# Kernel tuning notes

Measured on AMD Instinct MI355X. Metric: run time of the kernel, lower is better.

The kernel has to match this reference:

```python
import jax, jax.numpy as jnp
import numpy as np

EPS = 1e-5
NUM_GROUPS = 32


def setup_inputs() -> dict:
    key = jax.random.key(0)
    B, C, H, W = 16, 512, 32, 32
    ks = jax.random.split(key, 5)
    s = 1.0 / np.sqrt(C)  # keep attention logits well-scaled
    return {
        "x": jax.random.normal(ks[0], (B, C, H, W), jnp.float32),
        "gamma": jnp.ones((C,), jnp.float32),
        "beta": jnp.zeros((C,), jnp.float32),
        "wq": jax.random.normal(ks[1], (C, C), jnp.float32) * s,
        "bq": jnp.zeros((C,), jnp.float32),
        "wk": jax.random.normal(ks[2], (C, C), jnp.float32) * s,
        "bk": jnp.zeros((C,), jnp.float32),
        "wv": jax.random.normal(ks[3], (C, C), jnp.float32) * s,
        "bv": jnp.zeros((C,), jnp.float32),
        "wp": jax.random.normal(ks[4], (C, C), jnp.float32) * s,
        "bp": jnp.zeros((C,), jnp.float32),
    }


def _group_norm(x, gamma, beta):
    B, C, H, W = x.shape
    g = NUM_GROUPS
    xg = x.reshape(B, g, C // g, H * W)
    mu = jnp.mean(xg, axis=(2, 3), keepdims=True)
    var = jnp.mean(jnp.square(xg - mu), axis=(2, 3), keepdims=True)
    h = (xg - mu) * jax.lax.rsqrt(var + EPS)
    h = h.reshape(B, C, H, W)
    return h * gamma[None, :, None, None] + beta[None, :, None, None]


def reference(x, gamma, beta, wq, bq, wk, bk, wv, bv, wp, bp):
    B, C, H, W = x.shape
    N = H * W
    h = _group_norm(x, gamma, beta).reshape(B, C, N)  # [B,C,N]
    # 1x1 convs == per-pixel matmuls over channels
    q = jnp.einsum('oc,bcn->bon', wq, h) + bq[None, :, None]
    k = jnp.einsum('oc,bcn->bon', wk, h) + bk[None, :, None]
    v = jnp.einsum('oc,bcn->bon', wv, h) + bv[None, :, None]
    scale = int(C) ** (-0.5)
    logits = jnp.einsum('bcn,bcm->bnm', q, k) * scale  # [B,N,N]
    attn = jax.nn.softmax(logits, axis=-1)
    o = jnp.einsum('bnm,bcm->bcn', attn, v)  # [B,C,N]
    out = jnp.einsum('oc,bcn->bon', wp, o) + bp[None, :, None]
    return x + out.reshape(B, C, H, W)
```

## Files before the change

### kernel.cpp

```cpp
#include <hip/hip_runtime.h>
#include <hip/hip_bf16.h>

typedef __attribute__((ext_vector_type(8))) short bf16x8;
typedef __attribute__((ext_vector_type(4))) float f32x4;
typedef __attribute__((ext_vector_type(8))) unsigned short u16x8;
typedef __attribute__((ext_vector_type(4))) unsigned short u16x4;

static __device__ __forceinline__ unsigned short f2bf(float f) {
  __hip_bfloat16 h = __float2bfloat16(f);
  union { __hip_bfloat16 h; unsigned short u; } cv; cv.h = h; return cv.u;
}
static __device__ __forceinline__ float bf2f(unsigned short u) {
  union { unsigned int u; float f; } cv; cv.u = ((unsigned int)u) << 16; return cv.f;
}

static __device__ __forceinline__ void gload16(const unsigned short* g, unsigned short* l) {
  __builtin_amdgcn_global_load_lds((const __attribute__((address_space(1))) void*)g,
                                   (__attribute__((address_space(3))) void*)l, 16, 0, 0);
}

#define BK 32

__global__ __launch_bounds__(256, 4) void gemm_bt(
    const unsigned short* __restrict__ A, const unsigned short* __restrict__ Bm,
    long sA, long sB, int lda, int ldb, int K,
    const float* __restrict__ bias, int bias_mode, float post_scale,
    unsigned short* __restrict__ D, long sD, int ldd)
{
  __shared__ unsigned short lA[2][128 * BK];
  __shared__ unsigned short lB[2][128 * BK];
  const int gx = gridDim.x, gy = gridDim.y;
  const int nwg = gx * gy * gridDim.z;
  int orig = blockIdx.x + gx * (blockIdx.y + gy * blockIdx.z);
  int id = (orig & 7) * (nwg >> 3) + (orig >> 3);
  const int bxi = id % gx;
  int rem = id / gx;
  const int byi = rem % gy;
  const int bz = rem / gy;

  const int tid = threadIdx.x, lane = tid & 63, wid = tid >> 6;
  const int l15 = lane & 15, lhi = lane >> 4;
  const int wr = wid >> 1, wc = wid & 1;
  const long bm = (long)byi * 128, bn = (long)bxi * 128;
  const unsigned short* Ab = A + (size_t)bz * sA + (size_t)bm * lda;
  const unsigned short* Bb = Bm + (size_t)bz * sB + (size_t)bn * ldb;
  const int NT = K >> 5;

  f32x4 acc[4][4];
  #pragma unroll
  for (int i = 0; i < 4; ++i)
    #pragma unroll
    for (int j = 0; j < 4; ++j) acc[i][j] = (f32x4){0.f, 0.f, 0.f, 0.f};

  auto stage = [&](int buf, int k0) {
    #pragma unroll
    for (int j = 0; j < 2; ++j) {
      int bi = j * 256 + tid;
      int row = bi >> 2, sl = bi & 3;
      int kb = sl ^ ((row >> 1) & 3);
      gload16(Ab + (size_t)row * lda + k0 + kb * 8, &lA[buf][(j * 256 + wid * 64) * 8]);
    }
    #pragma unroll
    for (int j = 0; j < 2; ++j) {
      int bi = j * 256 + tid;
      int row = bi >> 2, sl = bi & 3;
      int kb = sl ^ ((row >> 1) & 3);
      gload16(Bb + (size_t)row * ldb + k0 + kb * 8, &lB[buf][(j * 256 + wid * 64) * 8]);
    }
  };

  stage(0, 0);
  __syncthreads();
  int buf = 0;
  for (int t = 0; t < NT; ++t) {
    if (t + 1 < NT) stage(buf ^ 1, (t + 1) * BK);
    bf16x8 af[4], bfr[4];
    #pragma unroll
    for (int mi = 0; mi < 4; ++mi) {
      int row = wr * 64 + mi * 16 + l15;
      int sl = lhi ^ ((row >> 1) & 3);
      af[mi] = *(const bf16x8*)&lA[buf][row * BK + sl * 8];
    }
    #pragma unroll
    for (int ni = 0; ni < 4; ++ni) {
      int row = wc * 64 + ni * 16 + l15;
      int sl = lhi ^ ((row >> 1) & 3);
      bfr[ni] = *(const bf16x8*)&lB[buf][row * BK + sl * 8];
    }
    #pragma unroll
    for (int mi = 0; mi < 4; ++mi)
      #pragma unroll
      for (int ni = 0; ni < 4; ++ni)
        acc[mi][ni] = __builtin_amdgcn_mfma_f32_16x16x32_bf16(af[mi], bfr[ni], acc[mi][ni], 0, 0, 0);
    __syncthreads();
    buf ^= 1;
  }

  #pragma unroll
  for (int mi = 0; mi < 4; ++mi) {
    #pragma unroll
    for (int ni = 0; ni < 4; ++ni) {
      #pragma unroll
      for (int r = 0; r < 4; ++r) {
        long row = bm + wr * 64 + mi * 16 + lhi * 4 + r;
        long col = bn + wc * 64 + ni * 16 + l15;
        float v = acc[mi][ni][r];
        if (bias_mode == 1) v += bias[row];
        else if (bias_mode == 2) v += bias[col];
        v *= post_scale;
        D[(size_t)bz * sD + (size_t)row * ldd + col] = f2bf(v);
      }
    }
  }
}

__global__ __launch_bounds__(256) void groupnorm_to_ht(
    const float* __restrict__ x, const float* __restrict__ gamma,
    const float* __restrict__ beta, unsigned short* __restrict__ ht)
{
  const int b = blockIdx.x >> 5;
  const int g = blockIdx.x & 31;
  const int tid = threadIdx.x, lane = tid & 63, wid = tid >> 6;
  const float4* xg4 = (const float4*)(x + ((size_t)b * 512 + g * 16) * 1024);
  float4 v[16];
  float s = 0.f, ss = 0.f;
  #pragma unroll
  for (int j = 0; j < 16; ++j) {
    v[j] = xg4[j * 256 + tid];
    s += v[j].x + v[j].y + v[j].z + v[j].w;
    ss += v[j].x * v[j].x + v[j].y * v[j].y + v[j].z * v[j].z + v[j].w * v[j].w;
  }
  #pragma unroll
  for (int o = 32; o; o >>= 1) { s += __shfl_xor(s, o); ss += __shfl_xor(ss, o); }
  __shared__ float red[8];
  if (lane == 0) { red[wid] = s; red[4 + wid] = ss; }
  __syncthreads();
  s = red[0] + red[1] + red[2] + red[3];
  ss = red[4] + red[5] + red[6] + red[7];
  const float mu = s * (1.f / 16384.f);
  const float var = ss * (1.f / 16384.f) - mu * mu;
  const float rsig = rsqrtf(var + 1e-5f);
  __shared__ unsigned short tile[16][1024];
  #pragma unroll
  for (int j = 0; j < 16; ++j) {
    int e = (j * 256 + tid) * 4;
    int ci = e >> 10, n = e & 1023;
    float ga = gamma[g * 16 + ci] * rsig, be = beta[g * 16 + ci];
    u16x4 o = { f2bf((v[j].x - mu) * ga + be), f2bf((v[j].y - mu) * ga + be),
                f2bf((v[j].z - mu) * ga + be), f2bf((v[j].w - mu) * ga + be) };
    *(u16x4*)&tile[ci][n] = o;
  }
  __syncthreads();
  unsigned short* hb = ht + (size_t)b * 1024 * 512 + g * 16;
  for (int rep = 0; rep < 4; ++rep) {
    int n = rep * 256 + tid;
    u16x8 lo, hi;
    #pragma unroll
    for (int ci = 0; ci < 8; ++ci) lo[ci] = tile[ci][n];
    #pragma unroll
    for (int ci = 0; ci < 8; ++ci) hi[ci] = tile[8 + ci][n];
    *(u16x8*)&hb[(size_t)n * 512] = lo;
    *(u16x8*)&hb[(size_t)n * 512 + 8] = hi;
  }
}

__global__ __launch_bounds__(256) void softmax_rows(unsigned short* __restrict__ attn)
{
  int row = blockIdx.x * 4 + (threadIdx.x >> 6);
  int lane = threadIdx.x & 63;
  unsigned short* p = attn + (size_t)row * 1024;
  u16x8 c0 = *(const u16x8*)&p[lane * 8];
  u16x8 c1 = *(const u16x8*)&p[512 + lane * 8];
  float f[16];
  #pragma unroll
  for (int j = 0; j < 8; ++j) { f[j] = bf2f(c0[j]); f[8 + j] = bf2f(c1[j]); }
  float m = f[0];
  #pragma unroll
  for (int j = 1; j < 16; ++j) m = fmaxf(m, f[j]);
  #pragma unroll
  for (int o = 32; o; o >>= 1) m = fmaxf(m, __shfl_xor(m, o));
  float sum = 0.f;
  #pragma unroll
  for (int j = 0; j < 16; ++j) { f[j] = __expf(f[j] - m); sum += f[j]; }
  #pragma unroll
  for (int o = 32; o; o >>= 1) sum += __shfl_xor(sum, o);
  float inv = 1.0f / sum;
  #pragma unroll
  for (int j = 0; j < 8; ++j) { c0[j] = f2bf(f[j] * inv); c1[j] = f2bf(f[8 + j] * inv); }
  *(u16x8*)&p[lane * 8] = c0;
  *(u16x8*)&p[512 + lane * 8] = c1;
}

__global__ __launch_bounds__(256) void residual_add(
    const float* __restrict__ x, const unsigned short* __restrict__ po,
    float* __restrict__ out)
{
  int t = blockIdx.x * 256 + threadIdx.x;
  int idx = t * 8;
  int b = idx >> 19, c = (idx >> 10) & 511, n = idx & 1023;
  u16x8 g = *(const u16x8*)&po[(size_t)c * 16384 + b * 1024 + n];
  float4 x0 = *(const float4*)&x[idx];
  float4 x1 = *(const float4*)&x[idx + 4];
  float4 o0 = { x0.x + bf2f(g[0]), x0.y + bf2f(g[1]), x0.z + bf2f(g[2]), x0.w + bf2f(g[3]) };
  float4 o1 = { x1.x + bf2f(g[4]), x1.y + bf2f(g[5]), x1.z + bf2f(g[6]), x1.w + bf2f(g[7]) };
  *(float4*)&out[idx] = o0;
  *(float4*)&out[idx + 4] = o1;
}

__global__ __launch_bounds__(256) void convert_weights(
    const float* __restrict__ wq, const float* __restrict__ wk,
    const float* __restrict__ wv, const float* __restrict__ wp,
    const float* __restrict__ bq, const float* __restrict__ bk,
    unsigned short* __restrict__ out, float* __restrict__ bqk)
{
  if (blockIdx.x == 1024) {
    int i = threadIdx.x * 4;
    if (i < 512) *(float4*)&bqk[i] = *(const float4*)&bq[i];
    else         *(float4*)&bqk[i] = *(const float4*)&bk[i - 512];
    return;
  }
  int t = blockIdx.x * 256 + threadIdx.x;
  int m = t >> 16;
  int off = (t & 65535) * 4;
  const float* src = m == 0 ? wq : m == 1 ? wk : m == 2 ? wv : wp;
  float4 v = *(const float4*)&src[off];
  u16x4 o = { f2bf(v.x), f2bf(v.y), f2bf(v.z), f2bf(v.w) };
  *(u16x4*)&out[(size_t)m * 262144 + off] = o;
}

extern "C" void kernel_launch(void* const* d_in, const int* in_sizes, int n_in,
                              void* d_out, int out_size, void* d_ws, size_t ws_size,
                              hipStream_t stream)
{
  const float* x     = (const float*)d_in[0];
  const float* gamma = (const float*)d_in[1];
  const float* beta  = (const float*)d_in[2];
  const float* wq    = (const float*)d_in[3];
  const float* bq    = (const float*)d_in[4];
  const float* wk    = (const float*)d_in[5];
  const float* bk    = (const float*)d_in[6];
  const float* wv    = (const float*)d_in[7];
  const float* bv    = (const float*)d_in[8];
  const float* wp    = (const float*)d_in[9];
  const float* bp    = (const float*)d_in[10];

  unsigned short* ws   = (unsigned short*)d_ws;
  unsigned short* w_bf = ws;
  unsigned short* ht   = w_bf + 1048576;
  unsigned short* qk   = ht + 8388608;
  unsigned short* vv2  = qk + 16777216;
  unsigned short* attn = vv2 + 8388608;
  unsigned short* ot   = attn + 16777216;
  float*          bqk  = (float*)(ot + 8388608);
  unsigned short* po   = attn;

  const float scale = 0.044194173824159216f;

  convert_weights<<<dim3(1025), dim3(256), 0, stream>>>(wq, wk, wv, wp, bq, bk, w_bf, bqk);
  groupnorm_to_ht<<<dim3(512), dim3(256), 0, stream>>>(x, gamma, beta, ht);

  gemm_bt<<<dim3(8, 128, 1), dim3(256), 0, stream>>>(
      ht, w_bf, 0L, 0L, 512, 512, 512,
      bqk, 2, 1.0f, qk, 0L, 1024);
  gemm_bt<<<dim3(128, 4, 1), dim3(256), 0, stream>>>(
      w_bf + 2 * 262144, ht, 0L, 0L, 512, 512, 512,
      bv, 1, 1.0f, vv2, 0L, 16384);
  gemm_bt<<<dim3(8, 8, 16), dim3(256), 0, stream>>>(
      qk, qk + 512, 1048576L, 1048576L, 1024, 1024, 512,
      (const float*)nullptr, 0, scale, attn, 1048576L, 1024);
  softmax_rows<<<dim3(4096), dim3(256), 0, stream>>>(attn);
  gemm_bt<<<dim3(4, 8, 16), dim3(256), 0, stream>>>(
      attn, vv2, 1048576L, 1024L, 1024, 16384, 1024,
      (const float*)nullptr, 0, 1.0f, ot, 524288L, 512);
  gemm_bt<<<dim3(128, 4, 1), dim3(256), 0, stream>>>(
      w_bf + 3 * 262144, ot, 0L, 0L, 512, 512, 512,
      bp, 1, 1.0f, po, 0L, 16384);
  residual_add<<<dim3(4096), dim3(256), 0, stream>>>(x, po, (float*)d_out);
}
```

Baseline: 185.7 us.

## Deepen GEMM pipeline to 4 stages, stage epilogue via LDS, fuse residual

The GEMM moves from a double-buffered LDS pipeline to a 4-slot ring in dynamic shared memory (64 KB), keeping three tiles in flight. It uses explicit vmcnt waits with a single barrier per iteration, aiming to hide global-load latency. Outputs are first staged through LDS so global stores are coalesced 16-byte writes. The final projection GEMM writes fp32 output with the residual added directly, which removes the separate residual_add kernel and the bf16 round-trip of the projection output. The larger LDS footprint lowers occupancy (launch bounds drop to 2 blocks per CU), and the hand-counted vmcnt values are fragile.

```diff
diff --git a/kernel.cpp b/kernel.cpp
--- a/kernel.cpp
+++ b/kernel.cpp
@@ -20,15 +20,16 @@
 }
 
 #define BK 32
-
-__global__ __launch_bounds__(256, 4) void gemm_bt(
+#define EPW 134
+
+__global__ __launch_bounds__(256, 2) void gemm_bt(
     const unsigned short* __restrict__ A, const unsigned short* __restrict__ Bm,
     long sA, long sB, int lda, int ldb, int K,
     const float* __restrict__ bias, int bias_mode, float post_scale,
-    unsigned short* __restrict__ D, long sD, int ldd)
-{
-  __shared__ unsigned short lA[2][128 * BK];
-  __shared__ unsigned short lB[2][128 * BK];
+    int out_mode, void* __restrict__ D, long sD, int ldd,
+    const float* __restrict__ resid)
+{
+  extern __shared__ unsigned short smem[];
   const int gx = gridDim.x, gy = gridDim.y;
   const int nwg = gx * gy * gridDim.z;
   int orig = blockIdx.x + gx * (blockIdx.y + gy * blockIdx.z);
@@ -52,64 +53,117 @@
     #pragma unroll
     for (int j = 0; j < 4; ++j) acc[i][j] = (f32x4){0.f, 0.f, 0.f, 0.f};
 
-  auto stage = [&](int buf, int k0) {
+  auto stage = [&](int t) {
+    const int slot = t & 3;
+    const int k0 = t * BK;
     #pragma unroll
     for (int j = 0; j < 2; ++j) {
       int bi = j * 256 + tid;
       int row = bi >> 2, sl = bi & 3;
       int kb = sl ^ ((row >> 1) & 3);
-      gload16(Ab + (size_t)row * lda + k0 + kb * 8, &lA[buf][(j * 256 + wid * 64) * 8]);
+      gload16(Ab + (size_t)row * lda + k0 + kb * 8,
+              &smem[slot * 8192 + (j * 256 + wid * 64) * 8]);
     }
     #pragma unroll
     for (int j = 0; j < 2; ++j) {
       int bi = j * 256 + tid;
       int row = bi >> 2, sl = bi & 3;
       int kb = sl ^ ((row >> 1) & 3);
-      gload16(Bb + (size_t)row * ldb + k0 + kb * 8, &lB[buf][(j * 256 + wid * 64) * 8]);
+      gload16(Bb + (size_t)row * ldb + k0 + kb * 8,
+              &smem[slot * 8192 + 4096 + (j * 256 + wid * 64) * 8]);
     }
   };
 
-  stage(0, 0);
-  __syncthreads();
-  int buf = 0;
+  stage(0); stage(1); stage(2);
+
   for (int t = 0; t < NT; ++t) {
-    if (t + 1 < NT) stage(buf ^ 1, (t + 1) * BK);
+    const int ahead = NT - 1 - t;
+    if (ahead >= 2)      asm volatile("s_waitcnt vmcnt(8)" ::: "memory");
+    else if (ahead == 1) asm volatile("s_waitcnt vmcnt(4)" ::: "memory");
+    else                 asm volatile("s_waitcnt vmcnt(0)" ::: "memory");
+    asm volatile("s_waitcnt lgkmcnt(0)" ::: "memory");
+    __builtin_amdgcn_s_barrier();
+    asm volatile("" ::: "memory");
+
+    const int slot = t & 3;
     bf16x8 af[4], bfr[4];
     #pragma unroll
     for (int mi = 0; mi < 4; ++mi) {
       int row = wr * 64 + mi * 16 + l15;
       int sl = lhi ^ ((row >> 1) & 3);
-      af[mi] = *(const bf16x8*)&lA[buf][row * BK + sl * 8];
+      af[mi] = *(const bf16x8*)&smem[slot * 8192 + row * BK + sl * 8];
     }
     #pragma unroll
     for (int ni = 0; ni < 4; ++ni) {
       int row = wc * 64 + ni * 16 + l15;
       int sl = lhi ^ ((row >> 1) & 3);
-      bfr[ni] = *(const bf16x8*)&lB[buf][row * BK + sl * 8];
-    }
+      bfr[ni] = *(const bf16x8*)&smem[slot * 8192 + 4096 + row * BK + sl * 8];
+    }
+    if (t + 3 < NT) stage(t + 3);
     #pragma unroll
     for (int mi = 0; mi < 4; ++mi)
       #pragma unroll
       for (int ni = 0; ni < 4; ++ni)
         acc[mi][ni] = __builtin_amdgcn_mfma_f32_16x16x32_bf16(af[mi], bfr[ni], acc[mi][ni], 0, 0, 0);
+  }
+  __syncthreads();
+
+  if (out_mode == 0) {
+    #pragma unroll
+    for (int mi = 0; mi < 4; ++mi) {
+      #pragma unroll
+      for (int ni = 0; ni < 4; ++ni) {
+        #pragma unroll
+        for (int r = 0; r < 4; ++r) {
+          int rl = wr * 64 + mi * 16 + lhi * 4 + r;
+          int cl = wc * 64 + ni * 16 + l15;
+          float v = acc[mi][ni][r];
+          if (bias_mode == 1) v += bias[bm + rl];
+          else if (bias_mode == 2) v += bias[bn + cl];
+          v *= post_scale;
+          smem[rl * EPW + cl] = f2bf(v);
+        }
+      }
+    }
     __syncthreads();
-    buf ^= 1;
-  }
-
-  #pragma unroll
-  for (int mi = 0; mi < 4; ++mi) {
-    #pragma unroll
-    for (int ni = 0; ni < 4; ++ni) {
+    const int row = tid >> 1, hf = tid & 1;
+    unsigned short* dst = (unsigned short*)D + (size_t)bz * sD + (size_t)(bm + row) * ldd + bn + hf * 64;
+    const unsigned short* src = &smem[row * EPW + hf * 64];
+    #pragma unroll
+    for (int j = 0; j < 8; ++j) *(u16x8*)&dst[j * 8] = *(const u16x8*)&src[j * 8];
+  } else {
+    float* smf = (float*)smem;
+    float* outF = (float*)D;
+    #pragma unroll
+    for (int h = 0; h < 2; ++h) {
+      if (wr == h) {
+        #pragma unroll
+        for (int mi = 0; mi < 4; ++mi)
+          #pragma unroll
+          for (int ni = 0; ni < 4; ++ni)
+            #pragma unroll
+            for (int r = 0; r < 4; ++r) {
+              int rl = mi * 16 + lhi * 4 + r;
+              int cl = wc * 64 + ni * 16 + l15;
+              float v = acc[mi][ni][r];
+              if (bias_mode == 1) v += bias[bm + h * 64 + rl];
+              smf[rl * EPW + cl] = v * post_scale;
+            }
+      }
+      __syncthreads();
+      const int rl = tid >> 2, q = tid & 3;
+      const long rowg = bm + h * 64 + rl;
       #pragma unroll
-      for (int r = 0; r < 4; ++r) {
-        long row = bm + wr * 64 + mi * 16 + lhi * 4 + r;
-        long col = bn + wc * 64 + ni * 16 + l15;
-        float v = acc[mi][ni][r];
-        if (bias_mode == 1) v += bias[row];
-        else if (bias_mode == 2) v += bias[col];
-        v *= post_scale;
-        D[(size_t)bz * sD + (size_t)row * ldd + col] = f2bf(v);
+      for (int j = 0; j < 8; ++j) {
+        long col = bn + q * 32 + j * 4;
+        long b = col >> 10, n = col & 1023;
+        size_t oi = (size_t)b * 524288 + (size_t)rowg * 1024 + n;
+        float4 v = *(const float4*)&smf[rl * EPW + q * 32 + j * 4];
+        float4 xr = *(const float4*)&resid[oi];
+        float4 o = { v.x + xr.x, v.y + xr.y, v.z + xr.z, v.w + xr.w };
+        *(float4*)&outF[oi] = o;
       }
+      __syncthreads();
     }
   }
 }
@@ -189,22 +243,6 @@
   for (int j = 0; j < 8; ++j) { c0[j] = f2bf(f[j] * inv); c1[j] = f2bf(f[8 + j] * inv); }
   *(u16x8*)&p[lane * 8] = c0;
   *(u16x8*)&p[512 + lane * 8] = c1;
-}
-
-__global__ __launch_bounds__(256) void residual_add(
-    const float* __restrict__ x, const unsigned short* __restrict__ po,
-    float* __restrict__ out)
-{
-  int t = blockIdx.x * 256 + threadIdx.x;
-  int idx = t * 8;
-  int b = idx >> 19, c = (idx >> 10) & 511, n = idx & 1023;
-  u16x8 g = *(const u16x8*)&po[(size_t)c * 16384 + b * 1024 + n];
-  float4 x0 = *(const float4*)&x[idx];
-  float4 x1 = *(const float4*)&x[idx + 4];
-  float4 o0 = { x0.x + bf2f(g[0]), x0.y + bf2f(g[1]), x0.z + bf2f(g[2]), x0.w + bf2f(g[3]) };
-  float4 o1 = { x1.x + bf2f(g[4]), x1.y + bf2f(g[5]), x1.z + bf2f(g[6]), x1.w + bf2f(g[7]) };
-  *(float4*)&out[idx] = o0;
-  *(float4*)&out[idx + 4] = o1;
 }
 
 __global__ __launch_bounds__(256) void convert_weights(
@@ -252,28 +290,29 @@
   unsigned short* attn = vv2 + 8388608;
   unsigned short* ot   = attn + 16777216;
   float*          bqk  = (float*)(ot + 8388608);
-  unsigned short* po   = attn;
 
   const float scale = 0.044194173824159216f;
+  const int SMEM = 65536;
+  hipFuncSetAttribute(reinterpret_cast<const void*>(&gemm_bt),
+                      hipFuncAttributeMaxDynamicSharedMemorySize, SMEM);
 
   convert_weights<<<dim3(1025), dim3(256), 0, stream>>>(wq, wk, wv, wp, bq, bk, w_bf, bqk);
   groupnorm_to_ht<<<dim3(512), dim3(256), 0, stream>>>(x, gamma, beta, ht);
 
-  gemm_bt<<<dim3(8, 128, 1), dim3(256), 0, stream>>>(
+  gemm_bt<<<dim3(8, 128, 1), dim3(256), SMEM, stream>>>(
       ht, w_bf, 0L, 0L, 512, 512, 512,
-      bqk, 2, 1.0f, qk, 0L, 1024);
-  gemm_bt<<<dim3(128, 4, 1), dim3(256), 0, stream>>>(
+      bqk, 2, 1.0f, 0, (void*)qk, 0L, 1024, (const float*)nullptr);
+  gemm_bt<<<dim3(128, 4, 1), dim3(256), SMEM, stream>>>(
       w_bf + 2 * 262144, ht, 0L, 0L, 512, 512, 512,
-      bv, 1, 1.0f, vv2, 0L, 16384);
-  gemm_bt<<<dim3(8, 8, 16), dim3(256), 0, stream>>>(
+      bv, 1, 1.0f, 0, (void*)vv2, 0L, 16384, (const float*)nullptr);
+  gemm_bt<<<dim3(8, 8, 16), dim3(256), SMEM, stream>>>(
       qk, qk + 512, 1048576L, 1048576L, 1024, 1024, 512,
-      (const float*)nullptr, 0, scale, attn, 1048576L, 1024);
+      (const float*)nullptr, 0, scale, 0, (void*)attn, 1048576L, 1024, (const float*)nullptr);
   softmax_rows<<<dim3(4096), dim3(256), 0, stream>>>(attn);
-  gemm_bt<<<dim3(4, 8, 16), dim3(256), 0, stream>>>(
+  gemm_bt<<<dim3(4, 8, 16), dim3(256), SMEM, stream>>>(
       attn, vv2, 1048576L, 1024L, 1024, 16384, 1024,
-      (const float*)nullptr, 0, 1.0f, ot, 524288L, 512);
-  gemm_bt<<<dim3(128, 4, 1), dim3(256), 0, stream>>>(
+      (const float*)nullptr, 0, 1.0f, 0, (void*)ot, 524288L, 512, (const float*)nullptr);
+  gemm_bt<<<dim3(128, 4, 1), dim3(256), SMEM, stream>>>(
       w_bf + 3 * 262144, ot, 0L, 0L, 512, 512, 512,
-      bp, 1, 1.0f, po, 0L, 16384);
-  residual_add<<<dim3(4096), dim3(256), 0, stream>>>(x, po, (float*)d_out);
-}
+      bp, 1, 1.0f, 1, d_out, 0L, 16384, x);
+}
```

After: 206.1 us. 11.0% more time.

## Load GEMM MFMA fragments directly from global memory, bypassing LDS staging

Applied to the files above, without the earlier changes.

The GEMM kernel drops its double-buffered LDS staging and __syncthreads barriers. Each wave now loads its A/B bf16 fragments straight from global memory into registers, using a two-deep register ping-pong to overlap loads with MFMA. This removes LDS traffic and block-wide synchronization. The cost is that wave pairs sharing rows load the same data twice from global/L2, plus higher register pressure (occupancy hint lowered from 4 to 3). The loop also assumes an even K/32 tile count.

```diff
diff --git a/kernel.cpp b/kernel.cpp
--- a/kernel.cpp
+++ b/kernel.cpp
@@ -14,21 +14,12 @@
   union { unsigned int u; float f; } cv; cv.u = ((unsigned int)u) << 16; return cv.f;
 }
 
-static __device__ __forceinline__ void gload16(const unsigned short* g, unsigned short* l) {
-  __builtin_amdgcn_global_load_lds((const __attribute__((address_space(1))) void*)g,
-                                   (__attribute__((address_space(3))) void*)l, 16, 0, 0);
-}
-
-#define BK 32
-
-__global__ __launch_bounds__(256, 4) void gemm_bt(
+__global__ __launch_bounds__(256, 3) void gemm_bt(
     const unsigned short* __restrict__ A, const unsigned short* __restrict__ Bm,
     long sA, long sB, int lda, int ldb, int K,
     const float* __restrict__ bias, int bias_mode, float post_scale,
     unsigned short* __restrict__ D, long sD, int ldd)
 {
-  __shared__ unsigned short lA[2][128 * BK];
-  __shared__ unsigned short lB[2][128 * BK];
   const int gx = gridDim.x, gy = gridDim.y;
   const int nwg = gx * gy * gridDim.z;
   int orig = blockIdx.x + gx * (blockIdx.y + gy * blockIdx.z);
@@ -42,9 +33,12 @@
   const int l15 = lane & 15, lhi = lane >> 4;
   const int wr = wid >> 1, wc = wid & 1;
   const long bm = (long)byi * 128, bn = (long)bxi * 128;
-  const unsigned short* Ab = A + (size_t)bz * sA + (size_t)bm * lda;
-  const unsigned short* Bb = Bm + (size_t)bz * sB + (size_t)bn * ldb;
-  const int NT = K >> 5;
+
+  const unsigned short* Abase = A + (size_t)bz * sA
+      + (size_t)(bm + wr * 64 + l15) * lda + lhi * 8;
+  const unsigned short* Bbase = Bm + (size_t)bz * sB
+      + (size_t)(bn + wc * 64 + l15) * ldb + lhi * 8;
+  const long lda16 = 16L * lda, ldb16 = 16L * ldb;
 
   f32x4 acc[4][4];
   #pragma unroll
@@ -52,48 +46,31 @@
     #pragma unroll
     for (int j = 0; j < 4; ++j) acc[i][j] = (f32x4){0.f, 0.f, 0.f, 0.f};
 
-  auto stage = [&](int buf, int k0) {
-    #pragma unroll
-    for (int j = 0; j < 2; ++j) {
-      int bi = j * 256 + tid;
-      int row = bi >> 2, sl = bi & 3;
-      int kb = sl ^ ((row >> 1) & 3);
-      gload16(Ab + (size_t)row * lda + k0 + kb * 8, &lA[buf][(j * 256 + wid * 64) * 8]);
-    }
-    #pragma unroll
-    for (int j = 0; j < 2; ++j) {
-      int bi = j * 256 + tid;
-      int row = bi >> 2, sl = bi & 3;
-      int kb = sl ^ ((row >> 1) & 3);
-      gload16(Bb + (size_t)row * ldb + k0 + kb * 8, &lB[buf][(j * 256 + wid * 64) * 8]);
-    }
+  bf16x8 a0[4], b0[4], a1[4], b1[4];
+
+  auto loadf = [&](bf16x8* af, bf16x8* bfr, int t) {
+    const unsigned short* ak = Abase + t * 32;
+    const unsigned short* bk = Bbase + t * 32;
+    #pragma unroll
+    for (int mi = 0; mi < 4; ++mi) af[mi] = *(const bf16x8*)(ak + mi * lda16);
+    #pragma unroll
+    for (int ni = 0; ni < 4; ++ni) bfr[ni] = *(const bf16x8*)(bk + ni * ldb16);
   };
-
-  stage(0, 0);
-  __syncthreads();
-  int buf = 0;
-  for (int t = 0; t < NT; ++t) {
-    if (t + 1 < NT) stage(buf ^ 1, (t + 1) * BK);
-    bf16x8 af[4], bfr[4];
-    #pragma unroll
-    for (int mi = 0; mi < 4; ++mi) {
-      int row = wr * 64 + mi * 16 + l15;
-      int sl = lhi ^ ((row >> 1) & 3);
-      af[mi] = *(const bf16x8*)&lA[buf][row * BK + sl * 8];
-    }
-    #pragma unroll
-    for (int ni = 0; ni < 4; ++ni) {
-      int row = wc * 64 + ni * 16 + l15;
-      int sl = lhi ^ ((row >> 1) & 3);
-      bfr[ni] = *(const bf16x8*)&lB[buf][row * BK + sl * 8];
-    }
+  auto fmaf = [&](bf16x8* af, bf16x8* bfr) {
     #pragma unroll
     for (int mi = 0; mi < 4; ++mi)
       #pragma unroll
       for (int ni = 0; ni < 4; ++ni)
         acc[mi][ni] = __builtin_amdgcn_mfma_f32_16x16x32_bf16(af[mi], bfr[ni], acc[mi][ni], 0, 0, 0);
-    __syncthreads();
-    buf ^= 1;
+  };
+
+  const int NT = K >> 5;
+  loadf(a0, b0, 0);
+  for (int t = 0; t + 2 <= NT; t += 2) {
+    loadf(a1, b1, t + 1);
+    fmaf(a0, b0);
+    if (t + 2 < NT) loadf(a0, b0, t + 2);
+    fmaf(a1, b1);
   }
 
   #pragma unroll
```

After: 342.4 us. 1.84x slower.

## Use single-buffered BK=64 GEMM tiles and fuse residual add into projection epilogue

Applied to the files above, without the earlier changes.

The GEMM kernel's K-tile grows from 32 to 64 and drops double buffering in favour of one LDS buffer with a stage-sync-compute-sync loop and an 8-way XOR swizzle. This halves the number of barriers per K but loses overlap between the global-to-LDS loads and the MFMA work. Separately, the output-projection GEMM gains an fp32 output mode that adds the residual x directly, removing the residual_add kernel and the bf16 intermediate round trip. The fused epilogue writes strided scalar fp32 values, so its stores may coalesce less well.

```diff
diff --git a/kernel.cpp b/kernel.cpp
--- a/kernel.cpp
+++ b/kernel.cpp
@@ -19,16 +19,17 @@
                                    (__attribute__((address_space(3))) void*)l, 16, 0, 0);
 }
 
-#define BK 32
+#define BK 64
 
 __global__ __launch_bounds__(256, 4) void gemm_bt(
     const unsigned short* __restrict__ A, const unsigned short* __restrict__ Bm,
     long sA, long sB, int lda, int ldb, int K,
     const float* __restrict__ bias, int bias_mode, float post_scale,
-    unsigned short* __restrict__ D, long sD, int ldd)
-{
-  __shared__ unsigned short lA[2][128 * BK];
-  __shared__ unsigned short lB[2][128 * BK];
+    int out_mode, void* __restrict__ D, long sD, int ldd,
+    const float* __restrict__ resid)
+{
+  __shared__ unsigned short lA[128 * BK];
+  __shared__ unsigned short lB[128 * BK];
   const int gx = gridDim.x, gy = gridDim.y;
   const int nwg = gx * gy * gridDim.z;
   int orig = blockIdx.x + gx * (blockIdx.y + gy * blockIdx.z);
@@ -44,7 +45,7 @@
   const long bm = (long)byi * 128, bn = (long)bxi * 128;
   const unsigned short* Ab = A + (size_t)bz * sA + (size_t)bm * lda;
   const unsigned short* Bb = Bm + (size_t)bz * sB + (size_t)bn * ldb;
-  const int NT = K >> 5;
+  const int NT = K >> 6;
 
   f32x4 acc[4][4];
   #pragma unroll
@@ -52,63 +53,83 @@
     #pragma unroll
     for (int j = 0; j < 4; ++j) acc[i][j] = (f32x4){0.f, 0.f, 0.f, 0.f};
 
-  auto stage = [&](int buf, int k0) {
-    #pragma unroll
-    for (int j = 0; j < 2; ++j) {
+  auto stage = [&](int k0) {
+    #pragma unroll
+    for (int j = 0; j < 4; ++j) {
       int bi = j * 256 + tid;
-      int row = bi >> 2, sl = bi & 3;
-      int kb = sl ^ ((row >> 1) & 3);
-      gload16(Ab + (size_t)row * lda + k0 + kb * 8, &lA[buf][(j * 256 + wid * 64) * 8]);
-    }
-    #pragma unroll
-    for (int j = 0; j < 2; ++j) {
+      int row = bi >> 3, sl = bi & 7;
+      int kb = sl ^ (row & 7);
+      gload16(Ab + (size_t)row * lda + k0 + kb * 8, &lA[(j * 256 + wid * 64) * 8]);
+    }
+    #pragma unroll
+    for (int j = 0; j < 4; ++j) {
       int bi = j * 256 + tid;
-      int row = bi >> 2, sl = bi & 3;
-      int kb = sl ^ ((row >> 1) & 3);
-      gload16(Bb + (size_t)row * ldb + k0 + kb * 8, &lB[buf][(j * 256 + wid * 64) * 8]);
+      int row = bi >> 3, sl = bi & 7;
+      int kb = sl ^ (row & 7);
+      gload16(Bb + (size_t)row * ldb + k0 + kb * 8, &lB[(j * 256 + wid * 64) * 8]);
     }
   };
 
-  stage(0, 0);
-  __syncthreads();
-  int buf = 0;
   for (int t = 0; t < NT; ++t) {
-    if (t + 1 < NT) stage(buf ^ 1, (t + 1) * BK);
-    bf16x8 af[4], bfr[4];
+    stage(t * BK);
+    __syncthreads();
+    #pragma unroll
+    for (int s = 0; s < 2; ++s) {
+      bf16x8 af[4], bfr[4];
+      #pragma unroll
+      for (int mi = 0; mi < 4; ++mi) {
+        int row = wr * 64 + mi * 16 + l15;
+        int sl = (s * 4 + lhi) ^ (row & 7);
+        af[mi] = *(const bf16x8*)&lA[row * BK + sl * 8];
+      }
+      #pragma unroll
+      for (int ni = 0; ni < 4; ++ni) {
+        int row = wc * 64 + ni * 16 + l15;
+        int sl = (s * 4 + lhi) ^ (row & 7);
+        bfr[ni] = *(const bf16x8*)&lB[row * BK + sl * 8];
+      }
+      #pragma unroll
+      for (int mi = 0; mi < 4; ++mi)
+        #pragma unroll
+        for (int ni = 0; ni < 4; ++ni)
+          acc[mi][ni] = __builtin_amdgcn_mfma_f32_16x16x32_bf16(af[mi], bfr[ni], acc[mi][ni], 0, 0, 0);
+    }
+    __syncthreads();
+  }
+
+  if (out_mode == 0) {
     #pragma unroll
     for (int mi = 0; mi < 4; ++mi) {
-      int row = wr * 64 + mi * 16 + l15;
-      int sl = lhi ^ ((row >> 1) & 3);
-      af[mi] = *(const bf16x8*)&lA[buf][row * BK + sl * 8];
-    }
-    #pragma unroll
-    for (int ni = 0; ni < 4; ++ni) {
-      int row = wc * 64 + ni * 16 + l15;
-      int sl = lhi ^ ((row >> 1) & 3);
-      bfr[ni] = *(const bf16x8*)&lB[buf][row * BK + sl * 8];
-    }
-    #pragma unroll
-    for (int mi = 0; mi < 4; ++mi)
-      #pragma unroll
-      for (int ni = 0; ni < 4; ++ni)
-        acc[mi][ni] = __builtin_amdgcn_mfma_f32_16x16x32_bf16(af[mi], bfr[ni], acc[mi][ni], 0, 0, 0);
-    __syncthreads();
-    buf ^= 1;
-  }
-
-  #pragma unroll
-  for (int mi = 0; mi < 4; ++mi) {
-    #pragma unroll
-    for (int ni = 0; ni < 4; ++ni) {
-      #pragma unroll
-      for (int r = 0; r < 4; ++r) {
-        long row = bm + wr * 64 + mi * 16 + lhi * 4 + r;
-        long col = bn + wc * 64 + ni * 16 + l15;
-        float v = acc[mi][ni][r];
-        if (bias_mode == 1) v += bias[row];
-        else if (bias_mode == 2) v += bias[col];
-        v *= post_scale;
-        D[(size_t)bz * sD + (size_t)row * ldd + col] = f2bf(v);
+      #pragma unroll
+      for (int ni = 0; ni < 4; ++ni) {
+        #pragma unroll
+        for (int r = 0; r < 4; ++r) {
+          long row = bm + wr * 64 + mi * 16 + lhi * 4 + r;
+          long col = bn + wc * 64 + ni * 16 + l15;
+          float v = acc[mi][ni][r];
+          if (bias_mode == 1) v += bias[row];
+          else if (bias_mode == 2) v += bias[col];
+          v *= post_scale;
+          ((unsigned short*)D)[(size_t)bz * sD + (size_t)row * ldd + col] = f2bf(v);
+        }
+      }
+    }
+  } else {
+    float* outF = (float*)D;
+    #pragma unroll
+    for (int mi = 0; mi < 4; ++mi) {
+      #pragma unroll
+      for (int ni = 0; ni < 4; ++ni) {
+        #pragma unroll
+        for (int r = 0; r < 4; ++r) {
+          long row = bm + wr * 64 + mi * 16 + lhi * 4 + r;
+          long col = bn + wc * 64 + ni * 16 + l15;
+          float v = acc[mi][ni][r];
+          if (bias_mode == 1) v += bias[row];
+          v *= post_scale;
+          size_t oi = (size_t)(col >> 10) * 524288 + (size_t)row * 1024 + (col & 1023);
+          outF[oi] = v + resid[oi];
+        }
       }
     }
   }
@@ -189,22 +210,6 @@
   for (int j = 0; j < 8; ++j) { c0[j] = f2bf(f[j] * inv); c1[j] = f2bf(f[8 + j] * inv); }
   *(u16x8*)&p[lane * 8] = c0;
   *(u16x8*)&p[512 + lane * 8] = c1;
-}
-
-__global__ __launch_bounds__(256) void residual_add(
-    const float* __restrict__ x, const unsigned short* __restrict__ po,
-    float* __restrict__ out)
-{
-  int t = blockIdx.x * 256 + threadIdx.x;
-  int idx = t * 8;
-  int b = idx >> 19, c = (idx >> 10) & 511, n = idx & 1023;
-  u16x8 g = *(const u16x8*)&po[(size_t)c * 16384 + b * 1024 + n];
-  float4 x0 = *(const float4*)&x[idx];
-  float4 x1 = *(const float4*)&x[idx + 4];
-  float4 o0 = { x0.x + bf2f(g[0]), x0.y + bf2f(g[1]), x0.z + bf2f(g[2]), x0.w + bf2f(g[3]) };
-  float4 o1 = { x1.x + bf2f(g[4]), x1.y + bf2f(g[5]), x1.z + bf2f(g[6]), x1.w + bf2f(g[7]) };
-  *(float4*)&out[idx] = o0;
-  *(float4*)&out[idx + 4] = o1;
 }
 
 __global__ __launch_bounds__(256) void convert_weights(
@@ -252,7 +257,6 @@
   unsigned short* attn = vv2 + 8388608;
   unsigned short* ot   = attn + 16777216;
   float*          bqk  = (float*)(ot + 8388608);
-  unsigned short* po   = attn;
 
   const float scale = 0.044194173824159216f;
 
@@ -261,19 +265,18 @@
 
   gemm_bt<<<dim3(8, 128, 1), dim3(256), 0, stream>>>(
       ht, w_bf, 0L, 0L, 512, 512, 512,
-      bqk, 2, 1.0f, qk, 0L, 1024);
+      bqk, 2, 1.0f, 0, (void*)qk, 0L, 1024, (const float*)nullptr);
   gemm_bt<<<dim3(128, 4, 1), dim3(256), 0, stream>>>(
       w_bf + 2 * 262144, ht, 0L, 0L, 512, 512, 512,
-      bv, 1, 1.0f, vv2, 0L, 16384);
+      bv, 1, 1.0f, 0, (void*)vv2, 0L, 16384, (const float*)nullptr);
   gemm_bt<<<dim3(8, 8, 16), dim3(256), 0, stream>>>(
       qk, qk + 512, 1048576L, 1048576L, 1024, 1024, 512,
-      (const float*)nullptr, 0, scale, attn, 1048576L, 1024);
+      (const float*)nullptr, 0, scale, 0, (void*)attn, 1048576L, 1024, (const float*)nullptr);
   softmax_rows<<<dim3(4096), dim3(256), 0, stream>>>(attn);
   gemm_bt<<<dim3(4, 8, 16), dim3(256), 0, stream>>>(
       attn, vv2, 1048576L, 1024L, 1024, 16384, 1024,
-      (const float*)nullptr, 0, 1.0f, ot, 524288L, 512);
+      (const float*)nullptr, 0, 1.0f, 0, (void*)ot, 524288L, 512, (const float*)nullptr);
   gemm_bt<<<dim3(128, 4, 1), dim3(256), 0, stream>>>(
       w_bf + 3 * 262144, ot, 0L, 0L, 512, 512, 512,
-      bp, 1, 1.0f, po, 0L, 16384);
-  residual_add<<<dim3(4096), dim3(256), 0, stream>>>(x, po, (float*)d_out);
-}
+      bp, 1, 1.0f, 1, d_out, 0L, 16384, x);
+}
```

Result: faster. 174.7 us (-5.9%).
